# Optimization experiments

Hardware: AMD Instinct MI355X
Metric: run time of the kernel (lower is better)

The kernel has to match this reference:

```python
import jax, jax.numpy as jnp
import numpy as np

N_EMBD = 1024
N_HEAD = 16
HEAD_DIM = N_EMBD // N_HEAD


def setup_inputs() -> dict:
    key = jax.random.key(0)
    k1, k2, k3, k4, k5 = jax.random.split(key, 5)
    B, T, C = 4, 2048, N_EMBD
    s = 0.02
    return {
        "x": jax.random.normal(k1, (B, T, C), dtype=jnp.float32),
        "w_qkv": jax.random.normal(k2, (C, 3 * C), dtype=jnp.float32) * s,
        "b_qkv": jnp.zeros((3 * C,), dtype=jnp.float32),
        "w_proj": jax.random.normal(k3, (C, C), dtype=jnp.float32) * s,
        "b_proj": jnp.zeros((C,), dtype=jnp.float32),
    }


def reference(x, w_qkv, b_qkv, w_proj, b_proj):
    B, T, C = x.shape
    H, D = N_HEAD, HEAD_DIM
    qkv = x @ w_qkv + b_qkv                      # [B,T,3C]
    q, k, v = jnp.split(qkv, 3, axis=2)
    q = q.reshape(B, T, H, D).transpose(0, 2, 1, 3)  # [B,H,T,D]
    k = k.reshape(B, T, H, D).transpose(0, 2, 1, 3)
    v = v.reshape(B, T, H, D).transpose(0, 2, 1, 3)
    att = jnp.einsum("bhqd,bhkd->bhqk", q, k) * (1.0 / D ** 0.5)
    causal = jnp.tril(jnp.ones((T, T), dtype=bool))
    att = jnp.where(causal[None, None], att, -jnp.inf)
    att = jax.nn.softmax(att, axis=-1)
    y = jnp.einsum("bhqk,bhkd->bhqd", att, v)    # [B,H,T,D]
    y = y.transpose(0, 2, 1, 3).reshape(B, T, C)
    return y @ w_proj + b_proj
```

## Files before the change

### kernel.cpp

```cpp
#include <hip/hip_runtime.h>
#include <hip/hip_bf16.h>

#define B_ 4
#define T_ 2048
#define C_ 1024
#define H_ 16
#define D_ 64
#define M_ (B_ * T_)
#define N3_ (3 * C_)

typedef __attribute__((ext_vector_type(4))) float f32x4;
typedef __attribute__((ext_vector_type(8))) short bf16x8;

__device__ __forceinline__ ushort f2bf(float f) {
  union { float f; unsigned u; } v; v.f = f;
  unsigned r = v.u + 0x7fffu + ((v.u >> 16) & 1u);
  return (ushort)(r >> 16);
}

__device__ __forceinline__ void gload_lds16(const ushort* g, ushort* l) {
  __builtin_amdgcn_global_load_lds((const __attribute__((address_space(1))) void*)g,
                                   (__attribute__((address_space(3))) void*)l, 16, 0, 0);
}

__global__ void cvt_bf16_kernel(const float* __restrict__ in, ushort* __restrict__ out, int n4) {
  int i = blockIdx.x * blockDim.x + threadIdx.x;
  int stride = gridDim.x * blockDim.x;
  for (; i < n4; i += stride) {
    float4 v = reinterpret_cast<const float4*>(in)[i];
    ushort4 o;
    o.x = f2bf(v.x); o.y = f2bf(v.y); o.z = f2bf(v.z); o.w = f2bf(v.w);
    reinterpret_cast<ushort4*>(out)[i] = o;
  }
}

__global__ __launch_bounds__(256) void transpose_cvt_kernel(const float* __restrict__ in,
                                                            ushort* __restrict__ out,
                                                            int K, int N) {
  __shared__ float tile[64][65];
  int k0 = blockIdx.y * 64, n0 = blockIdx.x * 64;
  int t = threadIdx.x;
  int rr = t >> 6, cc = t & 63;
#pragma unroll
  for (int i = 0; i < 16; ++i) {
    int r = i * 4 + rr;
    tile[r][cc] = in[(size_t)(k0 + r) * N + n0 + cc];
  }
  __syncthreads();
#pragma unroll
  for (int i = 0; i < 16; ++i) {
    int r = i * 4 + rr;
    out[(size_t)(n0 + r) * K + k0 + cc] = f2bf(tile[cc][r]);
  }
}

__global__ __launch_bounds__(256) void gemm_qkv_kernel(const ushort* __restrict__ A,
                                                       const ushort* __restrict__ Bt,
                                                       const float* __restrict__ bias,
                                                       ushort* __restrict__ qb,
                                                       ushort* __restrict__ kb,
                                                       ushort* __restrict__ vT) {
  __shared__ __align__(16) ushort As[128 * 32];
  __shared__ __align__(16) ushort Bs[128 * 32];
  const int tid = threadIdx.x;
  const int wid = tid >> 6, lane = tid & 63;
  const int wm = wid >> 1, wn = wid & 1;
  const int lr = lane & 15, lg = lane >> 4;
  const int bm = blockIdx.y * 128, bn = blockIdx.x * 128;
  const int srow = wid * 32 + (lane >> 2);
  const int scol = (lane & 3) * 8;
  ushort* lA = &As[wid * 32 * 32];
  ushort* lB = &Bs[wid * 32 * 32];
  const ushort* gA0 = A  + (size_t)(bm + srow) * 1024 + scol;
  const ushort* gB0 = Bt + (size_t)(bn + srow) * 1024 + scol;
  f32x4 acc[4][4] = {};
  for (int k0 = 0; k0 < 1024; k0 += 32) {
    gload_lds16(gA0 + k0, lA);
    gload_lds16(gA0 + k0 + 16 * 1024, lA + 16 * 32);
    gload_lds16(gB0 + k0, lB);
    gload_lds16(gB0 + k0 + 16 * 1024, lB + 16 * 32);
    __syncthreads();
    bf16x8 af[4], bfr[4];
#pragma unroll
    for (int f = 0; f < 4; ++f) {
      af[f]  = *(const bf16x8*)&As[(wm * 64 + f * 16 + lr) * 32 + lg * 8];
      bfr[f] = *(const bf16x8*)&Bs[(wn * 64 + f * 16 + lr) * 32 + lg * 8];
    }
#pragma unroll
    for (int fm = 0; fm < 4; ++fm)
#pragma unroll
      for (int fn = 0; fn < 4; ++fn)
        acc[fm][fn] = __builtin_amdgcn_mfma_f32_16x16x32_bf16(af[fm], bfr[fn], acc[fm][fn], 0, 0, 0);
    __syncthreads();
  }
#pragma unroll
  for (int fm = 0; fm < 4; ++fm)
#pragma unroll
    for (int fn = 0; fn < 4; ++fn) {
      int m0 = bm + wm * 64 + fm * 16 + lg * 4;
      int n  = bn + wn * 64 + fn * 16 + lr;
      float b = bias[n];
      int part = n >> 10, cch = n & 1023;
      int h = cch >> 6, d = cch & 63;
      int bb = m0 >> 11, t = m0 & 2047;
      size_t bh = (size_t)bb * H_ + h;
      if (part == 2) {
        ushort4 pv;
        pv.x = f2bf(acc[fm][fn][0] + b);
        pv.y = f2bf(acc[fm][fn][1] + b);
        pv.z = f2bf(acc[fm][fn][2] + b);
        pv.w = f2bf(acc[fm][fn][3] + b);
        *(ushort4*)&vT[(bh * D_ + d) * T_ + t] = pv;
      } else {
        ushort* dst = (part == 0) ? qb : kb;
#pragma unroll
        for (int r = 0; r < 4; ++r)
          dst[(bh * T_ + t + r) * D_ + d] = f2bf(acc[fm][fn][r] + b);
      }
    }
}

__global__ __launch_bounds__(256) void gemm_proj_kernel(const ushort* __restrict__ A,
                                                        const ushort* __restrict__ Bt,
                                                        const float* __restrict__ bias,
                                                        float* __restrict__ out) {
  __shared__ __align__(16) ushort As[128 * 32];
  __shared__ __align__(16) ushort Bs[128 * 32];
  const int tid = threadIdx.x;
  const int wid = tid >> 6, lane = tid & 63;
  const int wm = wid >> 1, wn = wid & 1;
  const int lr = lane & 15, lg = lane >> 4;
  const int bm = blockIdx.y * 128, bn = blockIdx.x * 128;
  const int srow = wid * 32 + (lane >> 2);
  const int scol = (lane & 3) * 8;
  ushort* lA = &As[wid * 32 * 32];
  ushort* lB = &Bs[wid * 32 * 32];
  const ushort* gA0 = A  + (size_t)(bm + srow) * 1024 + scol;
  const ushort* gB0 = Bt + (size_t)(bn + srow) * 1024 + scol;
  f32x4 acc[4][4] = {};
  for (int k0 = 0; k0 < 1024; k0 += 32) {
    gload_lds16(gA0 + k0, lA);
    gload_lds16(gA0 + k0 + 16 * 1024, lA + 16 * 32);
    gload_lds16(gB0 + k0, lB);
    gload_lds16(gB0 + k0 + 16 * 1024, lB + 16 * 32);
    __syncthreads();
    bf16x8 af[4], bfr[4];
#pragma unroll
    for (int f = 0; f < 4; ++f) {
      af[f]  = *(const bf16x8*)&As[(wm * 64 + f * 16 + lr) * 32 + lg * 8];
      bfr[f] = *(const bf16x8*)&Bs[(wn * 64 + f * 16 + lr) * 32 + lg * 8];
    }
#pragma unroll
    for (int fm = 0; fm < 4; ++fm)
#pragma unroll
      for (int fn = 0; fn < 4; ++fn)
        acc[fm][fn] = __builtin_amdgcn_mfma_f32_16x16x32_bf16(af[fm], bfr[fn], acc[fm][fn], 0, 0, 0);
    __syncthreads();
  }
#pragma unroll
  for (int fm = 0; fm < 4; ++fm)
#pragma unroll
    for (int fn = 0; fn < 4; ++fn)
#pragma unroll
      for (int r = 0; r < 4; ++r) {
        int m = bm + wm * 64 + fm * 16 + lg * 4 + r;
        int n = bn + wn * 64 + fn * 16 + lr;
        out[(size_t)m * C_ + n] = acc[fm][fn][r] + bias[n];
      }
}

__global__ __launch_bounds__(256) void attn_kernel(const ushort* __restrict__ qb,
                                                   const ushort* __restrict__ kb,
                                                   const ushort* __restrict__ vT,
                                                   ushort* __restrict__ yb) {
  __shared__ __align__(16) ushort Ks[64][72];
  __shared__ __align__(16) ushort Vs[64][72];
  __shared__ __align__(16) ushort Ps[4][16][72];
  const int bx = blockIdx.x, bh = blockIdx.y;
  const int tid = threadIdx.x, wid = tid >> 6, lane = tid & 63;
  const int lr = lane & 15, lg = lane >> 4;
  const ushort* Q  = qb + (size_t)bh * T_ * D_;
  const ushort* Kp = kb + (size_t)bh * T_ * D_;
  const ushort* Vp = vT + (size_t)bh * D_ * T_;
  const int bb = bh >> 4, h = bh & 15;

  for (int pass = 0; pass < 2; ++pass) {
    const int qt = pass == 0 ? bx : (T_ / 64 - 1) - bx;
    const int q0 = qt * 64;
    const int qw = q0 + wid * 16;
    bf16x8 qf[2];
    qf[0] = *(const bf16x8*)&Q[(size_t)(qw + lr) * D_ + lg * 8];
    qf[1] = *(const bf16x8*)&Q[(size_t)(qw + lr) * D_ + 32 + lg * 8];
    float mr[4], lsum[4];
    f32x4 o[4] = {};
#pragma unroll
    for (int r = 0; r < 4; ++r) { mr[r] = -1e30f; lsum[r] = 0.f; }
    for (int kt = 0; kt <= qt; ++kt) {
      int k0 = kt * 64;
#pragma unroll
      for (int p = 0; p < 2; ++p) {
        int idx = p * 256 + tid;
        int r = idx >> 3, c = (idx & 7) * 8;
        *(uint4*)&Ks[r][c] = *(const uint4*)&Kp[(size_t)(k0 + r) * D_ + c];
        *(uint4*)&Vs[r][c] = *(const uint4*)&Vp[(size_t)r * T_ + k0 + c];
      }
      __syncthreads();
      f32x4 s[4];
#pragma unroll
      for (int fk = 0; fk < 4; ++fk) {
        f32x4 a = {};
#pragma unroll
        for (int ks = 0; ks < 2; ++ks) {
          bf16x8 kf = *(const bf16x8*)&Ks[fk * 16 + lr][ks * 32 + lg * 8];
          a = __builtin_amdgcn_mfma_f32_16x16x32_bf16(qf[ks], kf, a, 0, 0, 0);
        }
#pragma unroll
        for (int r = 0; r < 4; ++r) s[fk][r] = a[r] * 0.125f;
      }
      if (kt == qt) {
#pragma unroll
        for (int fk = 0; fk < 4; ++fk)
#pragma unroll
          for (int r = 0; r < 4; ++r)
            if (k0 + fk * 16 + lr > qw + lg * 4 + r) s[fk][r] = -1e30f;
      }
#pragma unroll
      for (int r = 0; r < 4; ++r) {
        float v = fmaxf(fmaxf(s[0][r], s[1][r]), fmaxf(s[2][r], s[3][r]));
        v = fmaxf(v, __shfl_xor(v, 1));
        v = fmaxf(v, __shfl_xor(v, 2));
        v = fmaxf(v, __shfl_xor(v, 4));
        v = fmaxf(v, __shfl_xor(v, 8));
        float nm = fmaxf(mr[r], v);
        float sc = __expf(mr[r] - nm);
        mr[r] = nm;
        lsum[r] *= sc;
#pragma unroll
        for (int fd = 0; fd < 4; ++fd) o[fd][r] *= sc;
        float ps = 0.f;
#pragma unroll
        for (int fk = 0; fk < 4; ++fk) {
          float p = __expf(s[fk][r] - nm);
          s[fk][r] = p;
          ps += p;
        }
        ps += __shfl_xor(ps, 1);
        ps += __shfl_xor(ps, 2);
        ps += __shfl_xor(ps, 4);
        ps += __shfl_xor(ps, 8);
        lsum[r] += ps;
#pragma unroll
        for (int fk = 0; fk < 4; ++fk)
          Ps[wid][lg * 4 + r][fk * 16 + lr] = f2bf(s[fk][r]);
      }
      bf16x8 pa[2];
      pa[0] = *(const bf16x8*)&Ps[wid][lr][lg * 8];
      pa[1] = *(const bf16x8*)&Ps[wid][lr][32 + lg * 8];
#pragma unroll
      for (int fd = 0; fd < 4; ++fd)
#pragma unroll
        for (int ks = 0; ks < 2; ++ks) {
          bf16x8 vf = *(const bf16x8*)&Vs[fd * 16 + lr][ks * 32 + lg * 8];
          o[fd] = __builtin_amdgcn_mfma_f32_16x16x32_bf16(pa[ks], vf, o[fd], 0, 0, 0);
        }
      __syncthreads();
    }
#pragma unroll
    for (int fd = 0; fd < 4; ++fd)
#pragma unroll
      for (int r = 0; r < 4; ++r) {
        int t = qw + lg * 4 + r;
        float val = o[fd][r] / lsum[r];
        yb[((size_t)(bb * T_ + t)) * C_ + h * D_ + fd * 16 + lr] = f2bf(val);
      }
  }
}

extern "C" void kernel_launch(void* const* d_in, const int* in_sizes, int n_in,
                              void* d_out, int out_size, void* d_ws, size_t ws_size,
                              hipStream_t stream) {
  const float* x      = (const float*)d_in[0];
  const float* w_qkv  = (const float*)d_in[1];
  const float* b_qkv  = (const float*)d_in[2];
  const float* w_proj = (const float*)d_in[3];
  const float* b_proj = (const float*)d_in[4];
  float* out = (float*)d_out;

  char* ws = (char*)d_ws;
  const size_t MB = 1024 * 1024;
  ushort* xb     = (ushort*)(ws);
  ushort* wqkvT  = (ushort*)(ws + 16 * MB);
  ushort* wprojT = (ushort*)(ws + 22 * MB);
  ushort* qbuf   = (ushort*)(ws + 24 * MB);
  ushort* kbuf   = (ushort*)(ws + 40 * MB);
  ushort* vTbuf  = (ushort*)(ws + 56 * MB);
  ushort* ybuf   = (ushort*)(ws + 72 * MB);

  cvt_bf16_kernel<<<2048, 256, 0, stream>>>(x, xb, M_ * C_ / 4);
  transpose_cvt_kernel<<<dim3(N3_ / 64, C_ / 64), 256, 0, stream>>>(w_qkv, wqkvT, C_, N3_);
  transpose_cvt_kernel<<<dim3(C_ / 64, C_ / 64), 256, 0, stream>>>(w_proj, wprojT, C_, C_);
  gemm_qkv_kernel<<<dim3(N3_ / 128, M_ / 128), 256, 0, stream>>>(xb, wqkvT, b_qkv, qbuf, kbuf, vTbuf);
  attn_kernel<<<dim3(T_ / 128, B_ * H_), 256, 0, stream>>>(qbuf, kbuf, vTbuf, ybuf);
  gemm_proj_kernel<<<dim3(C_ / 128, M_ / 128), 256, 0, stream>>>(ybuf, wprojT, b_proj, out);
}
```

Baseline: 333.5 us.

## Rewrite attention with 32x32 MFMA, register-resident P, and lazy rescaling

```diff
diff --git a/kernel.cpp b/kernel.cpp
--- a/kernel.cpp
+++ b/kernel.cpp
@@ -10,6 +10,7 @@
 #define N3_ (3 * C_)
 
 typedef __attribute__((ext_vector_type(4))) float f32x4;
+typedef __attribute__((ext_vector_type(16))) float f32x16;
 typedef __attribute__((ext_vector_type(8))) short bf16x8;
 
 __device__ __forceinline__ ushort f2bf(float f) {
@@ -21,6 +22,12 @@
 __device__ __forceinline__ void gload_lds16(const ushort* g, ushort* l) {
   __builtin_amdgcn_global_load_lds((const __attribute__((address_space(1))) void*)g,
                                    (__attribute__((address_space(3))) void*)l, 16, 0, 0);
+}
+
+__device__ __forceinline__ unsigned cvtpk_bf16(float lo, float hi) {
+  unsigned r;
+  asm("v_cvt_pk_bf16_f32 %0, %1, %2" : "=v"(r) : "v"(lo), "v"(hi));
+  return r;
 }
 
 __global__ void cvt_bf16_kernel(const float* __restrict__ in, ushort* __restrict__ out, int n4) {
@@ -111,11 +118,14 @@
         pv.z = f2bf(acc[fm][fn][2] + b);
         pv.w = f2bf(acc[fm][fn][3] + b);
         *(ushort4*)&vT[(bh * D_ + d) * T_ + t] = pv;
+      } else if (part == 0) {
+#pragma unroll
+        for (int r = 0; r < 4; ++r)
+          qb[(bh * T_ + t + r) * D_ + d] = f2bf((acc[fm][fn][r] + b) * 0.125f);
       } else {
-        ushort* dst = (part == 0) ? qb : kb;
 #pragma unroll
         for (int r = 0; r < 4; ++r)
-          dst[(bh * T_ + t + r) * D_ + d] = f2bf(acc[fm][fn][r] + b);
+          kb[(bh * T_ + t + r) * D_ + d] = f2bf(acc[fm][fn][r] + b);
       }
     }
 }
@@ -169,110 +179,132 @@
       }
 }
 
-__global__ __launch_bounds__(256) void attn_kernel(const ushort* __restrict__ qb,
-                                                   const ushort* __restrict__ kb,
-                                                   const ushort* __restrict__ vT,
-                                                   ushort* __restrict__ yb) {
-  __shared__ __align__(16) ushort Ks[64][72];
-  __shared__ __align__(16) ushort Vs[64][72];
-  __shared__ __align__(16) ushort Ps[4][16][72];
-  const int bx = blockIdx.x, bh = blockIdx.y;
+__global__ void attn_kernel(const ushort* __restrict__ qb,
+                            const ushort* __restrict__ kb,
+                            const ushort* __restrict__ vT,
+                            ushort* __restrict__ yb) {
+  const int bh = blockIdx.y;
   const int tid = threadIdx.x, wid = tid >> 6, lane = tid & 63;
-  const int lr = lane & 15, lg = lane >> 4;
-  const ushort* Q  = qb + (size_t)bh * T_ * D_;
-  const ushort* Kp = kb + (size_t)bh * T_ * D_;
-  const ushort* Vp = vT + (size_t)bh * D_ * T_;
+  const int l31 = lane & 31, hi = lane >> 5;
+  const int wj = blockIdx.x * 4 + wid;
   const int bb = bh >> 4, h = bh & 15;
-
-  for (int pass = 0; pass < 2; ++pass) {
-    const int qt = pass == 0 ? bx : (T_ / 64 - 1) - bx;
-    const int q0 = qt * 64;
-    const int qw = q0 + wid * 16;
-    bf16x8 qf[2];
-    qf[0] = *(const bf16x8*)&Q[(size_t)(qw + lr) * D_ + lg * 8];
-    qf[1] = *(const bf16x8*)&Q[(size_t)(qw + lr) * D_ + 32 + lg * 8];
-    float mr[4], lsum[4];
-    f32x4 o[4] = {};
-#pragma unroll
-    for (int r = 0; r < 4; ++r) { mr[r] = -1e30f; lsum[r] = 0.f; }
-    for (int kt = 0; kt <= qt; ++kt) {
-      int k0 = kt * 64;
-#pragma unroll
-      for (int p = 0; p < 2; ++p) {
-        int idx = p * 256 + tid;
-        int r = idx >> 3, c = (idx & 7) * 8;
-        *(uint4*)&Ks[r][c] = *(const uint4*)&Kp[(size_t)(k0 + r) * D_ + c];
-        *(uint4*)&Vs[r][c] = *(const uint4*)&Vp[(size_t)r * T_ + k0 + c];
+  const ushort* Qb = qb + (size_t)bh * T_ * D_;
+  const ushort* Kb = kb + (size_t)bh * T_ * D_;
+  const ushort* Vb = vT + (size_t)bh * D_ * T_;
+  const ushort* V0 = Vb + (size_t)(0 * 32 + l31) * T_;
+  const ushort* V1 = Vb + (size_t)(1 * 32 + l31) * T_;
+
+  const int i = (blockIdx.z == 0) ? wj : 63 - wj;
+  const int qr0 = i * 32;
+  const int qrow = qr0 + l31;
+  const int ntiles = (i >> 1) + 1;
+  bf16x8 qf[4];
+#pragma unroll
+  for (int ds = 0; ds < 4; ++ds)
+    qf[ds] = *(const bf16x8*)&Qb[(size_t)qrow * D_ + ds * 16 + 8 * hi];
+  f32x16 o0 = {}, o1 = {};
+  float mrun = -1e30f, lsum = 0.f;
+
+  for (int tx = 0; tx < ntiles; ++tx) {
+    const int k0 = tx * 64;
+    bf16x8 kf0[4], kf1[4];
+#pragma unroll
+    for (int ds = 0; ds < 4; ++ds) {
+      kf0[ds] = *(const bf16x8*)&Kb[(size_t)(k0 + l31) * D_ + ds * 16 + 8 * hi];
+      kf1[ds] = *(const bf16x8*)&Kb[(size_t)(k0 + 32 + l31) * D_ + ds * 16 + 8 * hi];
+    }
+    bf16x8 vf0[4], vf1[4];
+#pragma unroll
+    for (int sl = 0; sl < 4; ++sl) {
+      vf0[sl] = *(const bf16x8*)&V0[k0 + sl * 16 + 8 * hi];
+      vf1[sl] = *(const bf16x8*)&V1[k0 + sl * 16 + 8 * hi];
+    }
+    f32x16 s0 = {}, s1 = {};
+#pragma unroll
+    for (int ds = 0; ds < 4; ++ds) {
+      s0 = __builtin_amdgcn_mfma_f32_32x32x16_bf16(kf0[ds], qf[ds], s0, 0, 0, 0);
+      s1 = __builtin_amdgcn_mfma_f32_32x32x16_bf16(kf1[ds], qf[ds], s1, 0, 0, 0);
+    }
+    if (tx == ntiles - 1) {
+#pragma unroll
+      for (int e = 0; e < 16; ++e) {
+        int key = k0 + (e & 3) + 8 * (e >> 2) + 4 * hi;
+        if (key > qrow)      s0[e] = -1e30f;
+        if (key + 32 > qrow) s1[e] = -1e30f;
       }
-      __syncthreads();
-      f32x4 s[4];
-#pragma unroll
-      for (int fk = 0; fk < 4; ++fk) {
-        f32x4 a = {};
-#pragma unroll
-        for (int ks = 0; ks < 2; ++ks) {
-          bf16x8 kf = *(const bf16x8*)&Ks[fk * 16 + lr][ks * 32 + lg * 8];
-          a = __builtin_amdgcn_mfma_f32_16x16x32_bf16(qf[ks], kf, a, 0, 0, 0);
-        }
-#pragma unroll
-        for (int r = 0; r < 4; ++r) s[fk][r] = a[r] * 0.125f;
+    }
+    float mx;
+    {
+      float a0 = fmaxf(fmaxf(s0[0], s0[1]), fmaxf(s0[2], s0[3]));
+      float a1 = fmaxf(fmaxf(s0[4], s0[5]), fmaxf(s0[6], s0[7]));
+      float a2 = fmaxf(fmaxf(s0[8], s0[9]), fmaxf(s0[10], s0[11]));
+      float a3 = fmaxf(fmaxf(s0[12], s0[13]), fmaxf(s0[14], s0[15]));
+      float b0 = fmaxf(fmaxf(s1[0], s1[1]), fmaxf(s1[2], s1[3]));
+      float b1 = fmaxf(fmaxf(s1[4], s1[5]), fmaxf(s1[6], s1[7]));
+      float b2 = fmaxf(fmaxf(s1[8], s1[9]), fmaxf(s1[10], s1[11]));
+      float b3 = fmaxf(fmaxf(s1[12], s1[13]), fmaxf(s1[14], s1[15]));
+      mx = fmaxf(fmaxf(fmaxf(a0, a1), fmaxf(a2, a3)), fmaxf(fmaxf(b0, b1), fmaxf(b2, b3)));
+    }
+    float pmax = fmaxf(mx, __shfl_xor(mx, 32));
+    if (!__all(pmax - mrun <= 8.f)) {
+      float nm = fmaxf(mrun, pmax);
+      float sc = __expf(mrun - nm);
+#pragma unroll
+      for (int e = 0; e < 16; ++e) { o0[e] *= sc; o1[e] *= sc; }
+      lsum *= sc;
+      mrun = nm;
+    }
+    float ls0 = 0.f, ls1 = 0.f, ls2 = 0.f, ls3 = 0.f;
+#pragma unroll
+    for (int e = 0; e < 4; ++e) {
+      s0[e]      = __expf(s0[e]      - mrun); ls0 += s0[e];
+      s0[e + 4]  = __expf(s0[e + 4]  - mrun); ls1 += s0[e + 4];
+      s0[e + 8]  = __expf(s0[e + 8]  - mrun); ls2 += s0[e + 8];
+      s0[e + 12] = __expf(s0[e + 12] - mrun); ls3 += s0[e + 12];
+    }
+#pragma unroll
+    for (int e = 0; e < 4; ++e) {
+      s1[e]      = __expf(s1[e]      - mrun); ls0 += s1[e];
+      s1[e + 4]  = __expf(s1[e + 4]  - mrun); ls1 += s1[e + 4];
+      s1[e + 8]  = __expf(s1[e + 8]  - mrun); ls2 += s1[e + 8];
+      s1[e + 12] = __expf(s1[e + 12] - mrun); ls3 += s1[e + 12];
+    }
+    lsum += (ls0 + ls1) + (ls2 + ls3);
+    bf16x8 pb[4];
+#pragma unroll
+    for (int half = 0; half < 2; ++half) {
+      const f32x16& sv = half == 0 ? s0 : s1;
+#pragma unroll
+      for (int ss = 0; ss < 2; ++ss) {
+        unsigned u = cvtpk_bf16(sv[ss * 8 + 0], sv[ss * 8 + 1]);
+        unsigned v = cvtpk_bf16(sv[ss * 8 + 2], sv[ss * 8 + 3]);
+        unsigned w = cvtpk_bf16(sv[ss * 8 + 4], sv[ss * 8 + 5]);
+        unsigned z = cvtpk_bf16(sv[ss * 8 + 6], sv[ss * 8 + 7]);
+        asm("v_permlane32_swap_b32 %0, %1" : "+v"(u), "+v"(w));
+        asm("v_permlane32_swap_b32 %0, %1" : "+v"(v), "+v"(z));
+        union { unsigned w4[4]; bf16x8 f; } pk;
+        pk.w4[0] = u; pk.w4[1] = v; pk.w4[2] = w; pk.w4[3] = z;
+        pb[half * 2 + ss] = pk.f;
       }
-      if (kt == qt) {
-#pragma unroll
-        for (int fk = 0; fk < 4; ++fk)
-#pragma unroll
-          for (int r = 0; r < 4; ++r)
-            if (k0 + fk * 16 + lr > qw + lg * 4 + r) s[fk][r] = -1e30f;
-      }
-#pragma unroll
-      for (int r = 0; r < 4; ++r) {
-        float v = fmaxf(fmaxf(s[0][r], s[1][r]), fmaxf(s[2][r], s[3][r]));
-        v = fmaxf(v, __shfl_xor(v, 1));
-        v = fmaxf(v, __shfl_xor(v, 2));
-        v = fmaxf(v, __shfl_xor(v, 4));
-        v = fmaxf(v, __shfl_xor(v, 8));
-        float nm = fmaxf(mr[r], v);
-        float sc = __expf(mr[r] - nm);
-        mr[r] = nm;
-        lsum[r] *= sc;
-#pragma unroll
-        for (int fd = 0; fd < 4; ++fd) o[fd][r] *= sc;
-        float ps = 0.f;
-#pragma unroll
-        for (int fk = 0; fk < 4; ++fk) {
-          float p = __expf(s[fk][r] - nm);
-          s[fk][r] = p;
-          ps += p;
-        }
-        ps += __shfl_xor(ps, 1);
-        ps += __shfl_xor(ps, 2);
-        ps += __shfl_xor(ps, 4);
-        ps += __shfl_xor(ps, 8);
-        lsum[r] += ps;
-#pragma unroll
-        for (int fk = 0; fk < 4; ++fk)
-          Ps[wid][lg * 4 + r][fk * 16 + lr] = f2bf(s[fk][r]);
-      }
-      bf16x8 pa[2];
-      pa[0] = *(const bf16x8*)&Ps[wid][lr][lg * 8];
-      pa[1] = *(const bf16x8*)&Ps[wid][lr][32 + lg * 8];
-#pragma unroll
-      for (int fd = 0; fd < 4; ++fd)
-#pragma unroll
-        for (int ks = 0; ks < 2; ++ks) {
-          bf16x8 vf = *(const bf16x8*)&Vs[fd * 16 + lr][ks * 32 + lg * 8];
-          o[fd] = __builtin_amdgcn_mfma_f32_16x16x32_bf16(pa[ks], vf, o[fd], 0, 0, 0);
-        }
-      __syncthreads();
-    }
-#pragma unroll
-    for (int fd = 0; fd < 4; ++fd)
-#pragma unroll
-      for (int r = 0; r < 4; ++r) {
-        int t = qw + lg * 4 + r;
-        float val = o[fd][r] / lsum[r];
-        yb[((size_t)(bb * T_ + t)) * C_ + h * D_ + fd * 16 + lr] = f2bf(val);
-      }
+    }
+#pragma unroll
+    for (int sl = 0; sl < 4; ++sl) {
+      o0 = __builtin_amdgcn_mfma_f32_32x32x16_bf16(vf0[sl], pb[sl], o0, 0, 0, 0);
+      o1 = __builtin_amdgcn_mfma_f32_32x32x16_bf16(vf1[sl], pb[sl], o1, 0, 0, 0);
+    }
+  }
+  float lt = lsum + __shfl_xor(lsum, 32);
+  float linv = 1.f / lt;
+  ushort* yrow = yb + ((size_t)(bb * T_ + qrow)) * C_ + h * D_;
+#pragma unroll
+  for (int rg = 0; rg < 4; ++rg) {
+    ushort4 w0, w1;
+    w0.x = f2bf(o0[rg * 4 + 0] * linv); w0.y = f2bf(o0[rg * 4 + 1] * linv);
+    w0.z = f2bf(o0[rg * 4 + 2] * linv); w0.w = f2bf(o0[rg * 4 + 3] * linv);
+    w1.x = f2bf(o1[rg * 4 + 0] * linv); w1.y = f2bf(o1[rg * 4 + 1] * linv);
+    w1.z = f2bf(o1[rg * 4 + 2] * linv); w1.w = f2bf(o1[rg * 4 + 3] * linv);
+    *(ushort4*)&yrow[8 * rg + 4 * hi]      = w0;
+    *(ushort4*)&yrow[32 + 8 * rg + 4 * hi] = w1;
   }
 }
 
@@ -300,6 +332,6 @@
   transpose_cvt_kernel<<<dim3(N3_ / 64, C_ / 64), 256, 0, stream>>>(w_qkv, wqkvT, C_, N3_);
   transpose_cvt_kernel<<<dim3(C_ / 64, C_ / 64), 256, 0, stream>>>(w_proj, wprojT, C_, C_);
   gemm_qkv_kernel<<<dim3(N3_ / 128, M_ / 128), 256, 0, stream>>>(xb, wqkvT, b_qkv, qbuf, kbuf, vTbuf);
-  attn_kernel<<<dim3(T_ / 128, B_ * H_), 256, 0, stream>>>(qbuf, kbuf, vTbuf, ybuf);
+  attn_kernel<<<dim3(8, B_ * H_, 2), 256, 0, stream>>>(qbuf, kbuf, vTbuf, ybuf);
   gemm_proj_kernel<<<dim3(C_ / 128, M_ / 128), 256, 0, stream>>>(ybuf, wprojT, b_proj, out);
 }
```

Measured after the change: 362.7 us. 1.09x slower.
